# Kernel tuning notes

Measured on AMD Instinct MI355X. Metric: run time of the kernel, lower is better.

Reference implementation:

```python
import jax, jax.numpy as jnp
import numpy as np

PC = 512      # proposal_channels == conv_channels
INCH = 512    # in_channels of branch
B = 8
T = 64        # pyramid level length (feat_t) at order=0
TF = 256      # frame_level_feature length (clip_length)
KERNELS = [8, 16, 8, 4, 2, 2, 2]  # ConPoolingKernal
CLC = 498     # feature_lastclass channels (CLC + 2 == 500)
GROUPS = 32


def _gn(x, gamma, beta):
    # GroupNorm(32, C) over [B, C, L]
    Bb, C, L = x.shape
    xg = x.reshape(Bb, GROUPS, C // GROUPS, L)
    m = xg.mean(axis=(2, 3), keepdims=True)
    v = xg.var(axis=(2, 3), keepdims=True)
    xn = ((xg - m) * jax.lax.rsqrt(v + 1e-5)).reshape(Bb, C, L)
    return xn * gamma[None, :, None] + beta[None, :, None]


def _c1(x, w, b):
    # Unit1D kernel_shape=1: pointwise conv
    return jnp.einsum('bct,oc->bot', x, w) + b[None, :, None]


def _bmp(feat, segs):
    # BoundaryMaxPooling: first C/2 channels max-pooled over segs[...,0:2],
    # second C/2 over segs[...,2:4] (inclusive integer ranges, clamped).
    Bb, C, L = feat.shape
    C2 = C // 2
    pos = jnp.arange(L)
    def pool(f, s, e):
        s = jnp.clip(s, 0, L - 1)
        e = jnp.maximum(jnp.clip(e, 0, L - 1), s)
        mask = (pos[None, None, :] >= s[..., None]) & (pos[None, None, :] <= e[..., None])  # [B,T,L]
        return jnp.max(jnp.where(mask[:, None], f[:, :, None, :], -jnp.inf), axis=-1)  # [B,C2,T]
    return jnp.concatenate([pool(feat[:, :C2], segs[..., 0], segs[..., 1]),
                            pool(feat[:, C2:], segs[..., 2], segs[..., 3])], axis=1)


def _anchor_gather(feat, anc, K):
    # Vectorized per-anchor clamp/slice + nearest F.interpolate(size=K):
    # src index for output k of a slice [l, r] is l + floor(k * (r - l + 1) / K).
    Bb, C, L = feat.shape
    left = jnp.clip(anc[..., 0], 0, L)
    right = jnp.clip(anc[..., 1], 0, L)
    valid = right > left                      # empty slices -> zeros (torch branch)
    seglen = right + 1 - left
    k = jnp.arange(K)
    idx = jnp.clip(left[..., None] + (k[None, None, :] * seglen[..., None]) // K, 0, L - 1)  # [B,T,K]
    g = jax.vmap(lambda f, ix: f[:, ix])(feat, idx)   # [B,C,T,K]
    return g * valid[:, None, :, None].astype(feat.dtype)


def setup_inputs() -> dict:
    key = jax.random.key(0)
    ks = jax.random.split(key, 16)
    f32 = jnp.float32
    s = 0.02
    def w(k, shape):
        return jax.random.normal(k, shape, f32) * s
    inp = {}
    inp['feature'] = jax.random.normal(ks[0], (B, INCH, T), f32)
    inp['frame_level_feature'] = jax.random.normal(ks[1], (B, PC, TF), f32)
    inp['segments'] = jax.random.randint(ks[2], (B, T, 4), 0, T).astype(jnp.int32)
    inp['frame_segments'] = jax.random.randint(ks[3], (B, T, 4), 0, TF).astype(jnp.int32)
    inp['feature_lastclass'] = jax.random.normal(ks[4], (B, CLC, T), f32)
    inp['anchor'] = jnp.sort(jax.random.randint(ks[5], (B, T, 2), 0, T), axis=-1).astype(jnp.int32)
    inp['frame_anchor'] = jnp.sort(jax.random.randint(ks[6], (B, T, 2), 0, TF), axis=-1).astype(jnp.int32)
    inp['order'] = 0
    inp['LocResult_feature'] = jax.random.normal(ks[7], (B, 2, T), f32)
    inp['w_cur'] = w(ks[8], (PC, INCH)); inp['b_cur'] = jnp.zeros((PC,), f32)
    inp['g_cur'] = jnp.ones((PC,), f32); inp['be_cur'] = jnp.zeros((PC,), f32)
    inp['w_lr'] = w(ks[9], (2 * PC, INCH)); inp['b_lr'] = jnp.zeros((2 * PC,), f32)
    inp['g_lr'] = jnp.ones((2 * PC,), f32); inp['be_lr'] = jnp.zeros((2 * PC,), f32)
    inp['w_roi'] = w(ks[10], (PC, PC)); inp['b_roi'] = jnp.zeros((PC,), f32)
    inp['g_roi'] = jnp.ones((PC,), f32); inp['be_roi'] = jnp.zeros((PC,), f32)
    K1 = KERNELS[1]; K0 = KERNELS[0]
    inp['w_cp'] = w(ks[11], (PC, 2 * PC, K1)); inp['b_cp'] = jnp.zeros((PC,), f32)
    inp['w_cp0'] = w(ks[12], (PC, PC, K0)); inp['b_cp0'] = jnp.zeros((PC,), f32)
    CIN = 6 * PC + 500
    inp['w_prop'] = w(ks[13], (INCH, CIN)); inp['b_prop'] = jnp.zeros((INCH,), f32)
    inp['g_prop'] = jnp.ones((INCH,), f32); inp['be_prop'] = jnp.zeros((INCH,), f32)
    return inp


def reference(feature, frame_level_feature, segments, frame_segments, feature_lastclass,
              anchor, frame_anchor, order, LocResult_feature,
              w_cur, b_cur, g_cur, be_cur, w_lr, b_lr, g_lr, be_lr,
              w_roi, b_roi, g_roi, be_roi, w_cp, b_cp, w_cp0, b_cp0,
              w_prop, b_prop, g_prop, be_prop):
    relu = jax.nn.relu
    fm_short = relu(_gn(_c1(feature, w_cur, b_cur), g_cur, be_cur))           # [B,PC,T]
    feat_lr = relu(_gn(_c1(feature, w_lr, b_lr), g_lr, be_lr))                # [B,2PC,T]
    prop_feature = _bmp(feat_lr, segments)                                    # [B,2PC,T]
    prop_roi = relu(_gn(_c1(_bmp(frame_level_feature, frame_segments), w_roi, b_roi), g_roi, be_roi))
    K1 = KERNELS[order + 1]
    K0 = KERNELS[0]
    g1 = _anchor_gather(feat_lr, anchor, K1)                                  # [B,2PC,T,K1]
    con_feature = jnp.einsum('bctk,ock->bot', g1, w_cp) + b_cp[None, :, None]  # valid conv K1->1
    g0 = _anchor_gather(frame_level_feature, frame_anchor, K0)                # [B,PC,T,K0]
    frame_con = jnp.einsum('bctk,ock->bot', g0, w_cp0) + b_cp0[None, :, None]
    prop_con = relu(_gn(_c1(frame_con, w_roi, b_roi), g_roi, be_roi))
    cat = jnp.concatenate([prop_roi, prop_feature, fm_short, feature_lastclass,
                           con_feature, prop_con, LocResult_feature], axis=1)  # [B,6PC+500,T]
    out = relu(_gn(_c1(cat, w_prop, b_prop), g_prop, be_prop))                # [B,INCH,T]
    return (out, feat_lr)
```

## Files before the change

kernel.cpp:

```cpp
#include <hip/hip_runtime.h>
#include <math.h>

#define BB 8
#define CATP 3584
#define CAT_REAL 3572

typedef __attribute__((ext_vector_type(8))) short short8;
typedef __attribute__((ext_vector_type(4))) float f32x4;

__device__ inline ushort f2bf(float f) {
  union { float f; unsigned u; } x;
  x.f = f;
  return (ushort)((x.u + 0x7FFFu + ((x.u >> 16) & 1u)) >> 16);
}
__device__ inline float bf2f(unsigned us) {
  union { unsigned u; float f; } x;
  x.u = us << 16;
  return x.f;
}

template <int Cin, int Kf>
__device__ void cpT_tile(const float* __restrict__ W, ushort* __restrict__ D,
                         int nt, int cc) {
  const int tid = threadIdx.x;
  const int j = tid >> 6, l4 = (tid >> 4) & 3, l15 = tid & 15;
  const int o = nt * 64 + j * 16 + l15;
  const int cb = cc * 32 + l4 * 8;
  ushort rg[8][Kf];
#pragma unroll
  for (int q = 0; q < 8; q++) {
    const float* row = W + ((size_t)o * Cin + cb + q) * Kf;
#pragma unroll
    for (int kq = 0; kq < Kf / 4; kq++) {
      const float4 f = *(const float4*)(row + kq * 4);
      rg[q][kq * 4 + 0] = f2bf(f.x);
      rg[q][kq * 4 + 1] = f2bf(f.y);
      rg[q][kq * 4 + 2] = f2bf(f.z);
      rg[q][kq * 4 + 3] = f2bf(f.w);
    }
  }
#pragma unroll
  for (int k = 0; k < Kf; k++) {
    uint4 pk;
    pk.x = (unsigned)rg[0][k] | ((unsigned)rg[1][k] << 16);
    pk.y = (unsigned)rg[2][k] | ((unsigned)rg[3][k] << 16);
    pk.z = (unsigned)rg[4][k] | ((unsigned)rg[5][k] << 16);
    pk.w = (unsigned)rg[6][k] | ((unsigned)rg[7][k] << 16);
    *(uint4*)(D + ((size_t)(nt * Kf + k) * (Cin >> 5) + cc) * 2048 + tid * 8) = pk;
  }
}

__global__ __launch_bounds__(256) void prep_kernel(
    const float* __restrict__ w_cur, const float* __restrict__ w_lr,
    const float* __restrict__ w_roi, const float* __restrict__ w_prop,
    ushort* __restrict__ Wcomb, ushort* __restrict__ Wroi,
    ushort* __restrict__ Wprop, const float* __restrict__ w_cp,
    ushort* __restrict__ WcpT, const float* __restrict__ w_cp0,
    ushort* __restrict__ Wcp0T, const float* __restrict__ feature,
    const float* __restrict__ frame_feat, const float* __restrict__ lastcls,
    const float* __restrict__ locres, ushort* __restrict__ Ft,
    ushort* __restrict__ FfT, ushort* __restrict__ cat) {
  __shared__ float tile[64 * 65];
  const int bid = blockIdx.x;
  if (bid < 1408) {
    const int i = bid * 256 + threadIdx.x;
    const float* src;
    ushort* dst;
    int o, k8, Kc;
    bool pad = false;
    if (i < 98304) {
      o = i >> 6; k8 = i & 63; Kc = 16;
      src = (o < 512) ? (w_cur + (size_t)o * 512)
                      : (w_lr + (size_t)(o - 512) * 512);
      dst = Wcomb;
    } else if (i < 131072) {
      const int r = i - 98304;
      o = r >> 6; k8 = r & 63; Kc = 16;
      src = w_roi + (size_t)o * 512;
      dst = Wroi;
    } else {
      const int r = i - 131072;
      if (r >= 229376) return;
      o = r / 448; k8 = r % 448; Kc = 112;
      src = w_prop + (size_t)o * CAT_REAL;
      dst = Wprop;
      pad = true;
    }
    const int k = k8 * 8;
    float v[8];
    if (pad) {
#pragma unroll
      for (int q = 0; q < 8; q++) v[q] = (k + q < CAT_REAL) ? src[k + q] : 0.f;
    } else {
      const float4 f0 = *(const float4*)(src + k);
      const float4 f1 = *(const float4*)(src + k + 4);
      v[0] = f0.x; v[1] = f0.y; v[2] = f0.z; v[3] = f0.w;
      v[4] = f1.x; v[5] = f1.y; v[6] = f1.z; v[7] = f1.w;
    }
    uint4 pk;
    pk.x = (unsigned)f2bf(v[0]) | ((unsigned)f2bf(v[1]) << 16);
    pk.y = (unsigned)f2bf(v[2]) | ((unsigned)f2bf(v[3]) << 16);
    pk.z = (unsigned)f2bf(v[4]) | ((unsigned)f2bf(v[5]) << 16);
    pk.w = (unsigned)f2bf(v[6]) | ((unsigned)f2bf(v[7]) << 16);
    const int ot = o >> 6, ii = (o >> 4) & 3, l15 = o & 15;
    const int kc = k8 >> 2, l4 = k8 & 3;
    const size_t flat =
        ((((size_t)ot * Kc + kc) * 4 + ii) * 64 + l4 * 16 + l15) * 8;
    *(uint4*)(dst + flat) = pk;
    return;
  }
  if (bid < 1792) {
    const int local = bid - 1408;
    if (local < 256)
      cpT_tile<1024, 16>(w_cp, WcpT, local >> 5, local & 31);
    else {
      const int r = local - 256;
      cpT_tile<512, 8>(w_cp0, Wcp0T, r >> 4, r & 15);
    }
    return;
  }
  const int local = bid - 1792;
  const float* src;
  ushort* dst;
  int Cr, Cw, L, rs, co, cblk, lblk, b;
  if (local < 64) {
    src = feature; dst = Ft; Cr = 512; Cw = 512; L = 64; rs = 512; co = 0;
    cblk = local & 7; lblk = 0; b = local >> 3;
  } else if (local < 320) {
    const int r = local - 64;
    src = frame_feat; dst = FfT; Cr = 512; Cw = 512; L = 256; rs = 512; co = 0;
    cblk = r & 7; lblk = (r >> 3) & 3; b = r >> 5;
  } else if (local < 384) {
    const int r = local - 320;
    src = lastcls; dst = cat; Cr = 498; Cw = 498; L = 64; rs = CATP; co = 2048;
    cblk = r & 7; lblk = 0; b = r >> 3;
  } else {
    const int r = local - 384;
    src = locres; dst = cat; Cr = 2; Cw = 14; L = 64; rs = CATP; co = 3570;
    cblk = 0; lblk = 0; b = r;
  }
  const int c0 = cblk * 64, l0 = lblk * 64;
  for (int e = threadIdx.x; e < 4096; e += 256) {
    const int cc = e >> 6, ll = e & 63;
    const int c = c0 + cc;
    tile[cc * 65 + ll] = (c < Cr) ? src[((size_t)b * Cr + c) * L + l0 + ll] : 0.f;
  }
  __syncthreads();
  for (int e = threadIdx.x; e < 4096; e += 256) {
    const int ll = e >> 6, cc = e & 63;
    const int c = c0 + cc;
    if (c < Cw)
      dst[((size_t)b * L + l0 + ll) * rs + co + c] = f2bf(tile[cc * 65 + ll]);
  }
}

__global__ __launch_bounds__(256) void gemm_gn_seg_kernel(
    int nblk0,
    const ushort* __restrict__ X0, const ushort* __restrict__ W0,
    const float* __restrict__ b0, const float* __restrict__ g0,
    const float* __restrict__ e0, int Kp0, int cs0, float* of0, int om0,
    ushort* co0, int cst0, int coff0,
    const ushort* __restrict__ X1, const ushort* __restrict__ W1,
    const float* __restrict__ b1, const float* __restrict__ g1,
    const float* __restrict__ e1, int Kp1, int cs1, float* of1, int om1,
    ushort* co1, int cst1, int coff1) {
  const int bx = blockIdx.x;
  const bool s1 = bx >= nblk0;
  const ushort* Xt = s1 ? X1 : X0;
  const ushort* Wb = s1 ? W1 : W0;
  const float* bias = s1 ? b1 : b0;
  const float* gamma = s1 ? g1 : g0;
  const float* beta = s1 ? e1 : e0;
  const int Kp = s1 ? Kp1 : Kp0;
  const int cpgShift = s1 ? cs1 : cs0;
  float* outF = s1 ? of1 : of0;
  const int outFM = s1 ? om1 : om0;
  ushort* catOut = s1 ? co1 : co0;
  const int catStride = s1 ? cst1 : cst0;
  const int chOff = s1 ? coff1 : coff0;
  const int o0 = (s1 ? bx - nblk0 : bx) * 64;

  const int b = blockIdx.y;
  const int w = threadIdx.x >> 6;
  const int lane = threadIdx.x & 63;
  const int l15 = lane & 15, l4 = lane >> 4;
  const int wk = Kp >> 2;
  const int kbeg = w * wk, kend = kbeg + wk;

  f32x4 acc[4][4] = {};
  const ushort* wbase = Wb + (size_t)(o0 >> 6) * (Kp >> 5) * 2048 + lane * 8;
  const ushort* bp[4];
#pragma unroll
  for (int j = 0; j < 4; j++)
    bp[j] = Xt + (size_t)(b * 64 + j * 16 + l15) * Kp + l4 * 8;

  for (int k = kbeg; k < kend; k += 32) {
    const int kc = k >> 5;
    short8 a[4], x[4];
#pragma unroll
    for (int i = 0; i < 4; i++)
      a[i] = *(const short8*)(wbase + ((size_t)kc * 4 + i) * 512);
#pragma unroll
    for (int j = 0; j < 4; j++) x[j] = *(const short8*)(bp[j] + k);
#pragma unroll
    for (int i = 0; i < 4; i++)
#pragma unroll
      for (int j = 0; j < 4; j++)
        acc[i][j] = __builtin_amdgcn_mfma_f32_16x16x32_bf16(a[i], x[j],
                                                            acc[i][j], 0, 0, 0);
  }

  __shared__ float red[64 * 65];
  for (int ww = 0; ww < 4; ww++) {
    __syncthreads();
    if (w == ww) {
#pragma unroll
      for (int i = 0; i < 4; i++)
#pragma unroll
        for (int j = 0; j < 4; j++)
#pragma unroll
          for (int r = 0; r < 4; r++) {
            const int m = i * 16 + l4 * 4 + r;
            const int n = j * 16 + l15;
            if (ww == 0)
              red[m * 65 + n] = acc[i][j][r] + bias[o0 + m];
            else
              red[m * 65 + n] += acc[i][j][r];
          }
    }
  }
  __syncthreads();

  const int cpg = 1 << cpgShift;
  const int ngroups = 64 >> cpgShift;
  __shared__ float rs[4], rss[4], gmean[4], grstd[4];
  for (int gi = 0; gi < ngroups; gi++) {
    float s = 0.f, ss = 0.f;
    const int nel = cpg << 6;
    for (int e = threadIdx.x; e < nel; e += 256) {
      const float v = red[((gi << cpgShift) + (e >> 6)) * 65 + (e & 63)];
      s += v;
      ss += v * v;
    }
#pragma unroll
    for (int off = 32; off > 0; off >>= 1) {
      s += __shfl_down(s, off);
      ss += __shfl_down(ss, off);
    }
    if (lane == 0) { rs[w] = s; rss[w] = ss; }
    __syncthreads();
    if (threadIdx.x == 0) {
      const float ts = rs[0] + rs[1] + rs[2] + rs[3];
      const float tss = rss[0] + rss[1] + rss[2] + rss[3];
      const float mean = ts / (float)nel;
      const float var = tss / (float)nel - mean * mean;
      gmean[gi] = mean;
      grstd[gi] = rsqrtf(var + 1e-5f);
    }
    __syncthreads();
  }

  if (outF) {
    for (int e = threadIdx.x; e < 4096; e += 256) {
      const int m = e >> 6, n = e & 63;
      const int gi = m >> cpgShift;
      const int c = o0 + m;
      float v = (red[m * 65 + n] - gmean[gi]) * grstd[gi] * gamma[c] + beta[c];
      v = fmaxf(v, 0.f);
      outF[((size_t)b * outFM + c) * 64 + n] = v;
    }
  }
  if (catOut) {
    for (int e = threadIdx.x; e < 4096; e += 256) {
      const int n = e >> 6, m = e & 63;
      const int gi = m >> cpgShift;
      const int c = o0 + m;
      float v = (red[m * 65 + n] - gmean[gi]) * grstd[gi] * gamma[c] + beta[c];
      v = fmaxf(v, 0.f);
      catOut[((size_t)(b * 64) + n) * catStride + chOff + c] = f2bf(v);
    }
  }
}

__global__ __launch_bounds__(256) void gemm_part_kernel(
    const ushort* __restrict__ Xt, const ushort* __restrict__ Wb,
    float* __restrict__ P) {
  const int b = blockIdx.x;
  const int ot = blockIdx.y;
  const int kz = blockIdx.z;
  const int w = threadIdx.x >> 6;
  const int lane = threadIdx.x & 63;
  const int l15 = lane & 15, l4 = lane >> 4;
  const int kbeg = kz * 896 + w * 224;
  const int kend = kbeg + 224;

  f32x4 acc[4][4] = {};
  const ushort* wbase = Wb + (size_t)ot * (CATP >> 5) * 2048 + lane * 8;
  const ushort* bp[4];
#pragma unroll
  for (int j = 0; j < 4; j++)
    bp[j] = Xt + (size_t)(b * 64 + j * 16 + l15) * CATP + l4 * 8;

  for (int k = kbeg; k < kend; k += 32) {
    const int kc = k >> 5;
    short8 a[4], x[4];
#pragma unroll
    for (int i = 0; i < 4; i++)
      a[i] = *(const short8*)(wbase + ((size_t)kc * 4 + i) * 512);
#pragma unroll
    for (int j = 0; j < 4; j++) x[j] = *(const short8*)(bp[j] + k);
#pragma unroll
    for (int i = 0; i < 4; i++)
#pragma unroll
      for (int j = 0; j < 4; j++)
        acc[i][j] = __builtin_amdgcn_mfma_f32_16x16x32_bf16(a[i], x[j],
                                                            acc[i][j], 0, 0, 0);
  }

  __shared__ float red[64 * 65];
  for (int ww = 0; ww < 4; ww++) {
    __syncthreads();
    if (w == ww) {
#pragma unroll
      for (int i = 0; i < 4; i++)
#pragma unroll
        for (int j = 0; j < 4; j++)
#pragma unroll
          for (int r = 0; r < 4; r++) {
            const int m = i * 16 + l4 * 4 + r;
            const int n = j * 16 + l15;
            if (ww == 0)
              red[m * 65 + n] = acc[i][j][r];
            else
              red[m * 65 + n] += acc[i][j][r];
          }
    }
  }
  __syncthreads();
  float* Pp = P + (((size_t)kz * BB + b) * 512 + ot * 64) * 64;
  for (int e = threadIdx.x; e < 4096; e += 256) Pp[e] = red[(e >> 6) * 65 + (e & 63)];
}

__global__ __launch_bounds__(256) void reduce_gn_kernel(
    const float* __restrict__ P, const float* __restrict__ bias,
    const float* __restrict__ gamma, const float* __restrict__ beta,
    float* __restrict__ outF) {
  const int ot = blockIdx.x;
  const int b = blockIdx.y;
  const int o0 = ot * 64;
  const int w = threadIdx.x >> 6;
  const int lane = threadIdx.x & 63;
  __shared__ float red[64 * 65];
  for (int e = threadIdx.x; e < 4096; e += 256) {
    const int m = e >> 6, n = e & 63;
    float s = bias[o0 + m];
#pragma unroll
    for (int z = 0; z < 4; z++)
      s += P[(((size_t)z * BB + b) * 512 + o0 + m) * 64 + n];
    red[m * 65 + n] = s;
  }
  __syncthreads();
  __shared__ float rs[4], rss[4], gmean[4], grstd[4];
  for (int gi = 0; gi < 4; gi++) {
    float s = 0.f, ss = 0.f;
    for (int e = threadIdx.x; e < 1024; e += 256) {
      const float v = red[((gi << 4) + (e >> 6)) * 65 + (e & 63)];
      s += v;
      ss += v * v;
    }
#pragma unroll
    for (int off = 32; off > 0; off >>= 1) {
      s += __shfl_down(s, off);
      ss += __shfl_down(ss, off);
    }
    if (lane == 0) { rs[w] = s; rss[w] = ss; }
    __syncthreads();
    if (threadIdx.x == 0) {
      const float ts = rs[0] + rs[1] + rs[2] + rs[3];
      const float tss = rss[0] + rss[1] + rss[2] + rss[3];
      const float mean = ts / 1024.f;
      const float var = tss / 1024.f - mean * mean;
      gmean[gi] = mean;
      grstd[gi] = rsqrtf(var + 1e-5f);
    }
    __syncthreads();
  }
  for (int e = threadIdx.x; e < 4096; e += 256) {
    const int m = e >> 6, n = e & 63;
    const int gi = m >> 4;
    const int c = o0 + m;
    float v = (red[m * 65 + n] - gmean[gi]) * grstd[gi] * gamma[c] + beta[c];
    outF[((size_t)b * 512 + c) * 64 + n] = fmaxf(v, 0.f);
  }
}

template <int C, int L>
__device__ void bmp_body(const ushort* __restrict__ Xt,
                         const int* __restrict__ segs, ushort* __restrict__ Y,
                         int rowStride, int chOff, float2 (*pmax)[512]) {
  constexpr int C2 = C / 2;
  constexpr int P2 = C2 / 2;
  constexpr int CH = P2 / 64;
  const int t = blockIdx.x;
  const int b = blockIdx.y;
  const int w = threadIdx.x >> 6;
  const int lane = threadIdx.x & 63;
  const int* sg = segs + ((size_t)b * 64 + t) * 4;
  const ushort* Xb = Xt + (size_t)b * L * C;
#pragma unroll
  for (int h = 0; h < 2; h++) {
    const int s = min(max(sg[2 * h], 0), L - 1);
    const int e = max(min(max(sg[2 * h + 1], 0), L - 1), s);
#pragma unroll
    for (int q = 0; q < CH; q++) {
      const int p = q * 64 + lane;
      const ushort* base = Xb + h * C2 + 2 * p;
      float a0 = -INFINITY, a1 = -INFINITY;
      float c0 = -INFINITY, c1 = -INFINITY;
      int l = s + w;
      for (; l + 4 <= e; l += 8) {
        const unsigned u0 = *(const unsigned*)(base + (size_t)l * C);
        const unsigned u1 = *(const unsigned*)(base + (size_t)(l + 4) * C);
        a0 = fmaxf(a0, bf2f(u0 & 0xffffu));
        a1 = fmaxf(a1, bf2f(u0 >> 16));
        c0 = fmaxf(c0, bf2f(u1 & 0xffffu));
        c1 = fmaxf(c1, bf2f(u1 >> 16));
      }
      if (l <= e) {
        const unsigned u0 = *(const unsigned*)(base + (size_t)l * C);
        a0 = fmaxf(a0, bf2f(u0 & 0xffffu));
        a1 = fmaxf(a1, bf2f(u0 >> 16));
      }
      pmax[w][h * P2 + p] = make_float2(fmaxf(a0, c0), fmaxf(a1, c1));
    }
  }
  __syncthreads();
  for (int idx = threadIdx.x; idx < 2 * P2; idx += 256) {
    float2 m = pmax[0][idx];
#pragma unroll
    for (int ww = 1; ww < 4; ww++) {
      const float2 v = pmax[ww][idx];
      m.x = fmaxf(m.x, v.x);
      m.y = fmaxf(m.y, v.y);
    }
    const unsigned o = (unsigned)f2bf(m.x) | ((unsigned)f2bf(m.y) << 16);
    *(unsigned*)(Y + ((size_t)(b * 64) + t) * rowStride + chOff + 2 * idx) = o;
  }
}

__global__ __launch_bounds__(256) void bmp_dual_kernel(
    const ushort* __restrict__ FlrT, const int* __restrict__ segments,
    ushort* __restrict__ cat, const ushort* __restrict__ FfT,
    const int* __restrict__ frame_segs, ushort* __restrict__ XbmpT) {
  __shared__ float2 pm[4][512];
  if (blockIdx.z == 0)
    bmp_body<1024, 64>(FlrT, segments, cat, CATP, 512, pm);
  else
    bmp_body<512, 256>(FfT, frame_segs, XbmpT, 512, 0, pm);
}

template <int Kf, int L, int Cin>
__device__ void anchor_mfma_body(const ushort* __restrict__ src,
                                 const int* __restrict__ anc,
                                 const ushort* __restrict__ Wt,
                                 float* __restrict__ P, int slice, float* red) {
  const int nt = blockIdx.x;
  const int b = blockIdx.y;
  const int w = threadIdx.x >> 6;
  const int lane = threadIdx.x & 63;
  const int l15 = lane & 15, l4 = lane >> 4;
  const int kz = slice >> 1, chalf = slice & 1;
  const int k = kz * 4 + w;
  const int cbase = chalf * (Cin / 2);

  const ushort* rp[4];
#pragma unroll
  for (int i = 0; i < 4; i++) {
    const int t = i * 16 + l15;
    const int a0 = anc[((size_t)b * 64 + t) * 2 + 0];
    const int a1 = anc[((size_t)b * 64 + t) * 2 + 1];
    const int left = min(max(a0, 0), L);
    const int right = min(max(a1, 0), L);
    const int seglen = right + 1 - left;
    const int ix = min(max(left + (k * seglen) / Kf, 0), L - 1);
    rp[i] = src + ((size_t)b * L + ix) * Cin + cbase + l4 * 8;
  }
  const ushort* wb = Wt + (size_t)(nt * Kf + k) * (Cin >> 5) * 2048 + lane * 8;

  f32x4 acc[4][4] = {};
  for (int c0 = 0; c0 < Cin / 2; c0 += 32) {
    const int cc = (cbase + c0) >> 5;
    short8 a[4], bb[4];
#pragma unroll
    for (int i = 0; i < 4; i++) a[i] = *(const short8*)(rp[i] + c0);
#pragma unroll
    for (int j = 0; j < 4; j++)
      bb[j] = *(const short8*)(wb + ((size_t)cc * 4 + j) * 512);
#pragma unroll
    for (int i = 0; i < 4; i++)
#pragma unroll
      for (int j = 0; j < 4; j++)
        acc[i][j] = __builtin_amdgcn_mfma_f32_16x16x32_bf16(a[i], bb[j],
                                                            acc[i][j], 0, 0, 0);
  }

  for (int ww = 0; ww < 4; ww++) {
    __syncthreads();
    if (w == ww) {
#pragma unroll
      for (int i = 0; i < 4; i++)
#pragma unroll
        for (int j = 0; j < 4; j++)
#pragma unroll
          for (int r = 0; r < 4; r++) {
            const int m = i * 16 + l4 * 4 + r;
            const int n = j * 16 + l15;
            if (ww == 0)
              red[m * 65 + n] = acc[i][j][r];
            else
              red[m * 65 + n] += acc[i][j][r];
          }
    }
  }
  __syncthreads();
  float* Pp = P + (((size_t)slice * BB + b) * 512 + nt * 64) * 64;
  for (int e = threadIdx.x; e < 4096; e += 256) {
    const int n = e >> 6, m = e & 63;
    Pp[e] = red[m * 65 + n];
  }
}

__global__ __launch_bounds__(256) void anchor_mfma_dual_kernel(
    const ushort* __restrict__ FlrT, const int* __restrict__ anchor,
    const ushort* __restrict__ WcpT, float* __restrict__ P1,
    const ushort* __restrict__ FfT, const int* __restrict__ frame_anchor,
    const ushort* __restrict__ Wcp0T, float* __restrict__ P0) {
  __shared__ float red[64 * 65];
  const int z = blockIdx.z;
  if (z < 8)
    anchor_mfma_body<16, 64, 1024>(FlrT, anchor, WcpT, P1, z, red);
  else
    anchor_mfma_body<8, 256, 512>(FfT, frame_anchor, Wcp0T, P0, z - 8, red);
}

__device__ void anchor_reduce_body(const float* __restrict__ P, int ks,
                                   const float* __restrict__ bias,
                                   const int* __restrict__ anc, int L,
                                   ushort* __restrict__ Y, int rowStride,
                                   int chOff, float* tile, float* sval) {
  const int o0 = blockIdx.x * 64;
  const int b = blockIdx.y;
  if (threadIdx.x < 64) {
    const int t = threadIdx.x;
    const int a0 = anc[((size_t)b * 64 + t) * 2 + 0];
    const int a1 = anc[((size_t)b * 64 + t) * 2 + 1];
    const int left = min(max(a0, 0), L);
    const int right = min(max(a1, 0), L);
    sval[t] = (right > left) ? 1.f : 0.f;
  }
  __syncthreads();
  for (int e = threadIdx.x; e < 4096; e += 256) {
    const int nl = e >> 6, m = e & 63;
    const int n = o0 + nl;
    float s = 0.f;
    for (int z = 0; z < ks; z++)
      s += P[(((size_t)z * BB + b) * 512 + n) * 64 + m];
    tile[nl * 65 + m] = s * sval[m] + bias[n];
  }
  __syncthreads();
  for (int e = threadIdx.x; e < 4096; e += 256) {
    const int m = e >> 6, nl = e & 63;
    Y[((size_t)(b * 64) + m) * rowStride + chOff + o0 + nl] =
        f2bf(tile[nl * 65 + m]);
  }
}

__global__ __launch_bounds__(256) void anchor_reduce_dual_kernel(
    const float* __restrict__ P1, const float* __restrict__ b_cp,
    const int* __restrict__ anchor, ushort* __restrict__ cat,
    const float* __restrict__ P0, const float* __restrict__ b_cp0,
    const int* __restrict__ frame_anchor, ushort* __restrict__ FconT) {
  __shared__ float tile[64 * 65];
  __shared__ float sval[64];
  if (blockIdx.z == 0)
    anchor_reduce_body(P1, 8, b_cp, anchor, 64, cat, CATP, 2546, tile, sval);
  else
    anchor_reduce_body(P0, 4, b_cp0, frame_anchor, 256, FconT, 512, 0, tile, sval);
}

extern "C" void kernel_launch(void* const* d_in, const int* in_sizes, int n_in,
                              void* d_out, int out_size, void* d_ws,
                              size_t ws_size, hipStream_t stream) {
  const float* feature      = (const float*)d_in[0];
  const float* frame_feat   = (const float*)d_in[1];
  const int*   segments     = (const int*)d_in[2];
  const int*   frame_segs   = (const int*)d_in[3];
  const float* feat_lastcls = (const float*)d_in[4];
  const int*   anchor       = (const int*)d_in[5];
  const int*   frame_anchor = (const int*)d_in[6];
  const float* locres       = (const float*)d_in[8];
  const float* w_cur  = (const float*)d_in[9];
  const float* b_cur  = (const float*)d_in[10];
  const float* g_cur  = (const float*)d_in[11];
  const float* be_cur = (const float*)d_in[12];
  const float* w_lr   = (const float*)d_in[13];
  const float* b_lr   = (const float*)d_in[14];
  const float* g_lr   = (const float*)d_in[15];
  const float* be_lr  = (const float*)d_in[16];
  const float* w_roi  = (const float*)d_in[17];
  const float* b_roi  = (const float*)d_in[18];
  const float* g_roi  = (const float*)d_in[19];
  const float* be_roi = (const float*)d_in[20];
  const float* w_cp   = (const float*)d_in[21];
  const float* b_cp   = (const float*)d_in[22];
  const float* w_cp0  = (const float*)d_in[23];
  const float* b_cp0  = (const float*)d_in[24];
  const float* w_prop = (const float*)d_in[25];
  const float* b_prop = (const float*)d_in[26];
  const float* g_prop = (const float*)d_in[27];
  const float* be_prop= (const float*)d_in[28];

  float* out_main = (float*)d_out;
  float* feat_lr  = (float*)d_out + BB * 512 * 64;

  ushort* cat_t  = (ushort*)d_ws;
  ushort* Ft     = cat_t + 1835008;
  ushort* XbmpT  = Ft + 262144;
  ushort* FconT  = XbmpT + 262144;
  ushort* Wcomb  = FconT + 262144;
  ushort* Wroi   = Wcomb + 786432;
  ushort* Wprop  = Wroi + 262144;
  ushort* WcpT   = Wprop + 1835008;
  ushort* Wcp0T  = WcpT + 8388608;
  ushort* FlrT   = Wcp0T + 2097152;
  ushort* FfT    = FlrT + 524288;
  float*  P1     = (float*)(FfT + 1048576);
  float*  P0     = P1 + 2097152;
  float*  P9     = P0 + 1048576;

  prep_kernel<<<2184, 256, 0, stream>>>(
      w_cur, w_lr, w_roi, w_prop, Wcomb, Wroi, Wprop, w_cp, WcpT, w_cp0,
      Wcp0T, feature, frame_feat, feat_lastcls, locres, Ft, FfT, cat_t);

  gemm_gn_seg_kernel<<<dim3(24, BB), 256, 0, stream>>>(
      8,
      Ft, Wcomb, b_cur, g_cur, be_cur, 512, 4, nullptr, 0, cat_t, CATP, 1536,
      Ft, Wcomb + 512 * 512, b_lr, g_lr, be_lr, 512, 5, feat_lr, 1024, FlrT,
      1024, 0);

  bmp_dual_kernel<<<dim3(64, BB, 2), 256, 0, stream>>>(
      FlrT, segments, cat_t, FfT, frame_segs, XbmpT);

  anchor_mfma_dual_kernel<<<dim3(8, BB, 12), 256, 0, stream>>>(
      FlrT, anchor, WcpT, P1, FfT, frame_anchor, Wcp0T, P0);

  anchor_reduce_dual_kernel<<<dim3(8, BB, 2), 256, 0, stream>>>(
      P1, b_cp, anchor, cat_t, P0, b_cp0, frame_anchor, FconT);

  gemm_gn_seg_kernel<<<dim3(16, BB), 256, 0, stream>>>(
      8,
      XbmpT, Wroi, b_roi, g_roi, be_roi, 512, 4, nullptr, 0, cat_t, CATP, 0,
      FconT, Wroi, b_roi, g_roi, be_roi, 512, 4, nullptr, 0, cat_t, CATP, 3058);

  gemm_part_kernel<<<dim3(BB, 8, 4), 256, 0, stream>>>(cat_t, Wprop, P9);

  reduce_gn_kernel<<<dim3(8, BB), 256, 0, stream>>>(
      P9, b_prop, g_prop, be_prop, out_main);
}
```

Measured before the change: 269.7 us.

## Stage conv-pooling weight transpose through LDS and split prep into two kernels

Result: slower. 277.4 us (+2.8%).

```diff
diff --git a/kernel.cpp b/kernel.cpp
--- a/kernel.cpp
+++ b/kernel.cpp
@@ -20,43 +20,78 @@
 }
 
 template <int Cin, int Kf>
-__device__ void cpT_tile(const float* __restrict__ W, ushort* __restrict__ D,
-                         int nt, int cc) {
+__device__ void cpT_lds(const float* __restrict__ W, ushort* __restrict__ D,
+                        int nt, int cc, unsigned* lds) {
+  constexpr int F4PO = 32 * Kf / 4;
+  constexpr int U32PO = 32 * Kf / 2;
+  constexpr int GSZ = 4 * Kf;
+  constexpr int NITER = 64 * F4PO / 256;
   const int tid = threadIdx.x;
+  for (int it = 0; it < NITER; ++it) {
+    const int f = it * 256 + tid;
+    const int o = f / F4PO;
+    const int r = f % F4PO;
+    const int cl = (r * 4) / Kf;
+    const int k0 = (r * 4) & (Kf - 1);
+    const float4 v =
+        *(const float4*)(W + ((size_t)(nt * 64 + o) * Cin + cc * 32) * Kf +
+                         r * 4);
+    const unsigned A = (unsigned)f2bf(v.x) | ((unsigned)f2bf(v.y) << 16);
+    const unsigned B = (unsigned)f2bf(v.z) | ((unsigned)f2bf(v.w) << 16);
+    const unsigned Ap = __shfl_xor(A, Kf / 4);
+    const unsigned Bp = __shfl_xor(B, Kf / 4);
+    if ((cl & 1) == 0) {
+      const int cp = cl >> 1;
+      const int g = cp >> 2;
+      const int cpl = cp & 3;
+      const int rot = o + g;
+      const int base = o * U32PO + g * GSZ;
+      const int l0 = cpl * Kf + k0;
+      const unsigned out0 = (A & 0xffffu) | ((Ap & 0xffffu) << 16);
+      const unsigned out1 = (A >> 16) | ((Ap >> 16) << 16);
+      const unsigned out2 = (B & 0xffffu) | ((Bp & 0xffffu) << 16);
+      const unsigned out3 = (B >> 16) | ((Bp >> 16) << 16);
+      lds[base + ((l0 + 0 + rot) & (GSZ - 1))] = out0;
+      lds[base + ((l0 + 1 + rot) & (GSZ - 1))] = out1;
+      lds[base + ((l0 + 2 + rot) & (GSZ - 1))] = out2;
+      lds[base + ((l0 + 3 + rot) & (GSZ - 1))] = out3;
+    }
+  }
+  __syncthreads();
   const int j = tid >> 6, l4 = (tid >> 4) & 3, l15 = tid & 15;
-  const int o = nt * 64 + j * 16 + l15;
-  const int cb = cc * 32 + l4 * 8;
-  ushort rg[8][Kf];
-#pragma unroll
-  for (int q = 0; q < 8; q++) {
-    const float* row = W + ((size_t)o * Cin + cb + q) * Kf;
-#pragma unroll
-    for (int kq = 0; kq < Kf / 4; kq++) {
-      const float4 f = *(const float4*)(row + kq * 4);
-      rg[q][kq * 4 + 0] = f2bf(f.x);
-      rg[q][kq * 4 + 1] = f2bf(f.y);
-      rg[q][kq * 4 + 2] = f2bf(f.z);
-      rg[q][kq * 4 + 3] = f2bf(f.w);
-    }
-  }
+  const int o = j * 16 + l15;
+  const int rot = o + l4;
+  const int base = o * U32PO + l4 * GSZ;
 #pragma unroll
   for (int k = 0; k < Kf; k++) {
     uint4 pk;
-    pk.x = (unsigned)rg[0][k] | ((unsigned)rg[1][k] << 16);
-    pk.y = (unsigned)rg[2][k] | ((unsigned)rg[3][k] << 16);
-    pk.z = (unsigned)rg[4][k] | ((unsigned)rg[5][k] << 16);
-    pk.w = (unsigned)rg[6][k] | ((unsigned)rg[7][k] << 16);
-    *(uint4*)(D + ((size_t)(nt * Kf + k) * (Cin >> 5) + cc) * 2048 + tid * 8) = pk;
-  }
-}
-
-__global__ __launch_bounds__(256) void prep_kernel(
+    pk.x = lds[base + ((0 * Kf + k + rot) & (GSZ - 1))];
+    pk.y = lds[base + ((1 * Kf + k + rot) & (GSZ - 1))];
+    pk.z = lds[base + ((2 * Kf + k + rot) & (GSZ - 1))];
+    pk.w = lds[base + ((3 * Kf + k + rot) & (GSZ - 1))];
+    *(uint4*)(D + ((size_t)(nt * Kf + k) * (Cin >> 5) + cc) * 2048 + tid * 8) =
+        pk;
+  }
+}
+
+__global__ __launch_bounds__(256) void prep_heavy_kernel(
+    const float* __restrict__ w_cp, ushort* __restrict__ WcpT,
+    const float* __restrict__ w_cp0, ushort* __restrict__ Wcp0T) {
+  __shared__ unsigned lds[64 * 256];
+  const int bid = blockIdx.x;
+  if (bid < 256)
+    cpT_lds<1024, 16>(w_cp, WcpT, bid >> 5, bid & 31, lds);
+  else {
+    const int r = bid - 256;
+    cpT_lds<512, 8>(w_cp0, Wcp0T, r >> 4, r & 15, lds);
+  }
+}
+
+__global__ __launch_bounds__(256) void prep_light_kernel(
     const float* __restrict__ w_cur, const float* __restrict__ w_lr,
     const float* __restrict__ w_roi, const float* __restrict__ w_prop,
     ushort* __restrict__ Wcomb, ushort* __restrict__ Wroi,
-    ushort* __restrict__ Wprop, const float* __restrict__ w_cp,
-    ushort* __restrict__ WcpT, const float* __restrict__ w_cp0,
-    ushort* __restrict__ Wcp0T, const float* __restrict__ feature,
+    ushort* __restrict__ Wprop, const float* __restrict__ feature,
     const float* __restrict__ frame_feat, const float* __restrict__ lastcls,
     const float* __restrict__ locres, ushort* __restrict__ Ft,
     ushort* __restrict__ FfT, ushort* __restrict__ cat) {
@@ -109,17 +144,7 @@
     *(uint4*)(dst + flat) = pk;
     return;
   }
-  if (bid < 1792) {
-    const int local = bid - 1408;
-    if (local < 256)
-      cpT_tile<1024, 16>(w_cp, WcpT, local >> 5, local & 31);
-    else {
-      const int r = local - 256;
-      cpT_tile<512, 8>(w_cp0, Wcp0T, r >> 4, r & 15);
-    }
-    return;
-  }
-  const int local = bid - 1792;
+  const int local = bid - 1408;
   const float* src;
   ushort* dst;
   int Cr, Cw, L, rs, co, cblk, lblk, b;
@@ -638,9 +663,11 @@
   float*  P0     = P1 + 2097152;
   float*  P9     = P0 + 1048576;
 
-  prep_kernel<<<2184, 256, 0, stream>>>(
-      w_cur, w_lr, w_roi, w_prop, Wcomb, Wroi, Wprop, w_cp, WcpT, w_cp0,
-      Wcp0T, feature, frame_feat, feat_lastcls, locres, Ft, FfT, cat_t);
+  prep_heavy_kernel<<<384, 256, 0, stream>>>(w_cp, WcpT, w_cp0, Wcp0T);
+
+  prep_light_kernel<<<1800, 256, 0, stream>>>(
+      w_cur, w_lr, w_roi, w_prop, Wcomb, Wroi, Wprop, feature, frame_feat,
+      feat_lastcls, locres, Ft, FfT, cat_t);
 
   gemm_gn_seg_kernel<<<dim3(24, BB), 256, 0, stream>>>(
       8,
```
